# Optimization experiments

Measured on AMD Instinct MI355X. Metric: run time of the kernel, lower is better.

The kernel has to match this reference:

```python
import jax, jax.numpy as jnp
import numpy as np
from math import sqrt

D = 512        # output_dim (layer_dims[-1])
H = 4          # num_heads
ATN = D // H   # atn_dim = 128
BERT_D = 768
B = 32         # number of graph pairs
NP = 4096
NH = 4096


def setup_inputs() -> dict:
    key = jax.random.key(0)
    ks = jax.random.split(key, 20)
    inp = {
        'ctx_p': jax.random.normal(ks[0], (NP, D), jnp.float32),
        'ctx_h': jax.random.normal(ks[1], (NH, D), jnp.float32),
        'lhs_p': jax.random.normal(ks[2], (NP, BERT_D), jnp.float32),
        'lhs_h': jax.random.normal(ks[3], (NH, BERT_D), jnp.float32),
        'batch_p': jnp.sort(jax.random.randint(ks[4], (NP,), 0, B)).astype(jnp.int64),
        'batch_h': jnp.sort(jax.random.randint(ks[5], (NH,), 0, B)).astype(jnp.int64),
        # learned parameters (stored [in, out])
        'Wq': jax.random.normal(ks[6], (D, D), jnp.float32) * 0.02,
        'bq': jnp.zeros((D,), jnp.float32),
        'Wk': jax.random.normal(ks[7], (D, D), jnp.float32) * 0.02,
        'bk': jnp.zeros((D,), jnp.float32),
        'Wv': jax.random.normal(ks[8], (BERT_D, BERT_D), jnp.float32) * 0.02,
        'bv': jnp.zeros((BERT_D,), jnp.float32),
        'W1': jax.random.normal(ks[9], (D + BERT_D, 256), jnp.float32) * 0.02,
        'b1': jnp.zeros((256,), jnp.float32),
        'W2': jax.random.normal(ks[10], (256, 128), jnp.float32) * 0.02,
        'ln_g': jnp.ones((128,), jnp.float32),
        'ln_b': jnp.zeros((128,), jnp.float32),
        'Wc': jax.random.normal(ks[11], (128, 3), jnp.float32) * 0.02,
        'bc': jnp.zeros((3,), jnp.float32),
    }
    return inp


def reference(ctx_p, ctx_h, lhs_p, lhs_h, batch_p, batch_h,
              Wq, bq, Wk, bk, Wv, bv, W1, b1, W2, ln_g, ln_b, Wc, bc):
    # q/k projections; torch code does .view(-1, atn_dim, num_heads) -> head is fastest axis
    qs = (ctx_h @ Wq + bq).reshape(-1, ATN, H)          # [nh, atn, H]
    ks = (ctx_p @ Wk + bk).reshape(-1, ATN, H)          # [np, atn, H]
    vs = (lhs_p @ Wv + bv).reshape(-1, H, BERT_D // H)  # [np, H, 768/H]

    atn = jnp.einsum('ndh,mdh->nmh', qs, ks) / sqrt(ATN)  # [nh, np, H]
    # faithful to original: positions where batch ids MATCH are set to -1e10
    mask_same = batch_h[:, None] == batch_p[None, :]       # [nh, np]
    atn = jnp.where(mask_same[:, :, None], jnp.float32(-1e10), atn)
    atn = jax.nn.softmax(atn, axis=1)                      # softmax over premise words m

    attended = jnp.einsum('nmh,mhd->nhd', atn, vs).reshape(-1, BERT_D)  # [nh, 768]

    feats = jnp.concatenate([ctx_h, lhs_h - attended], axis=1)  # [nh, D+768]
    h1 = jax.nn.gelu(feats @ W1 + b1, approximate=False)
    h2 = h1 @ W2                                                # Linear no bias
    mu = h2.mean(axis=-1, keepdims=True)
    var = ((h2 - mu) ** 2).mean(axis=-1, keepdims=True)
    h2 = (h2 - mu) * jax.lax.rsqrt(var + 1e-5) * ln_g + ln_b    # LayerNorm(128)

    # global_mean_pool over batch_h
    pooled = jax.ops.segment_sum(h2, batch_h, num_segments=B)
    counts = jax.ops.segment_sum(jnp.ones((h2.shape[0], 1), h2.dtype), batch_h, num_segments=B)
    pooled = pooled / jnp.maximum(counts, 1.0)

    return pooled @ Wc + bc  # [B, 3]
```

## Files before the change

kernel.cpp:

```cpp
#include <hip/hip_runtime.h>
#include <hip/hip_bf16.h>
#include <math.h>

#define NP_N 4096
#define NH_N 4096
#define D_N 512
#define BERT_N 768
#define H_N 4
#define B_N 32
#define SCL2 0.12754245006257576f

typedef __attribute__((ext_vector_type(8))) short short8;
typedef __attribute__((ext_vector_type(4))) float f32x4;
typedef __attribute__((ext_vector_type(4))) unsigned short ush4;
typedef __attribute__((ext_vector_type(4))) unsigned int uivec4;
typedef unsigned short ushort_t;

__device__ __forceinline__ void gl_lds16(const void* g, void* l) {
    __builtin_amdgcn_global_load_lds((const __attribute__((address_space(1))) void*)g,
                                     (__attribute__((address_space(3))) void*)l, 16, 0, 0);
}
__device__ __forceinline__ unsigned short f2bu(float f) {
    __hip_bfloat16 b = __float2bfloat16(f);
    return *reinterpret_cast<unsigned short*>(&b);
}
__device__ __forceinline__ float b2f(unsigned short u) {
    union { unsigned int i; float f; } x; x.i = ((unsigned int)u) << 16; return x.f;
}
__device__ __forceinline__ unsigned int pkbf(float a, float b) {
    union { __hip_bfloat162 h; unsigned int u; } x;
    x.h.x = __float2bfloat16(a);
    x.h.y = __float2bfloat16(b);
    return x.u;
}
__device__ __forceinline__ unsigned int sxor(unsigned int v, int m) {
    return (unsigned int)__shfl_xor((int)v, m);
}

__device__ __forceinline__ short8 mkfrag(uint2 u, uint2 v, bool hi, bool godd) {
    unsigned ux32 = sxor(u.x, 32), uy32 = sxor(u.y, 32);
    unsigned vx32 = sxor(v.x, 32), vy32 = sxor(v.y, 32);
    unsigned ax = hi ? vx32 : u.x, bx = hi ? v.x : ux32;
    unsigned ay = hi ? vy32 : u.y, by = hi ? v.y : uy32;
    unsigned sbx = sxor(bx, 16), sax = sxor(ax, 16);
    unsigned sby = sxor(by, 16), say = sxor(ay, 16);
    uivec4 w;
    w.x = godd ? sbx : ax;
    w.y = godd ? sby : ay;
    w.z = godd ? bx : sax;
    w.w = godd ? by : say;
    return __builtin_bit_cast(short8, w);
}

#define EW_BLOCKS 512
__global__ __launch_bounds__(256) void convert_all(
    const float* __restrict__ ctx_h, const float* __restrict__ ctx_p,
    const float* __restrict__ lhs_p,
    const float* __restrict__ Wq, const float* __restrict__ Wk,
    const float* __restrict__ Wv, const float* __restrict__ W1,
    const float* __restrict__ bq, const float* __restrict__ bk,
    ushort_t* __restrict__ ctxp_bf, ushort_t* __restrict__ lhsp_bf,
    ushort_t* __restrict__ feats,
    ushort_t* __restrict__ Wqt, ushort_t* __restrict__ Wkt,
    ushort_t* __restrict__ Wvt, ushort_t* __restrict__ W1t,
    float* __restrict__ bqp, float* __restrict__ bkp)
{
    const int bid = blockIdx.x, t = threadIdx.x;
    if (bid < EW_BLOCKS) {
        const long N0 = 524288, N1 = 1048576, TOT = 1835008;
        for (long i = (long)bid * 256 + t; i < TOT; i += (long)EW_BLOCKS * 256) {
            float4 v; ush4 o;
            if (i < N0) {
                long k = i;
                v = ((const float4*)ctx_h)[k];
                o[0] = f2bu(v.x); o[1] = f2bu(v.y); o[2] = f2bu(v.z); o[3] = f2bu(v.w);
                long n = k >> 7, c4 = k & 127;
                ((ush4*)feats)[n * 320 + c4] = o;
            } else if (i < N1) {
                long k = i - N0;
                v = ((const float4*)ctx_p)[k];
                o[0] = f2bu(v.x); o[1] = f2bu(v.y); o[2] = f2bu(v.z); o[3] = f2bu(v.w);
                ((ush4*)ctxp_bf)[k] = o;
            } else {
                long k = i - N1;
                v = ((const float4*)lhs_p)[k];
                o[0] = f2bu(v.x); o[1] = f2bu(v.y); o[2] = f2bu(v.z); o[3] = f2bu(v.w);
                ((ush4*)lhsp_bf)[k] = o;
            }
        }
        if (bid == 0) {
            for (int n = t; n < 512; n += 256) {
                int np = (n & 3) * 128 + (n >> 2);
                bqp[np] = bq[n] * SCL2;
                bkp[np] = bk[n];
            }
        }
        return;
    }
    int tb = bid - EW_BLOCKS;
    const float* src; ushort_t* dst; int K, N, tile, perm; float wscl;
    if (tb < 64)       { src = Wq; dst = Wqt; K = 512;  N = 512; tile = tb;       perm = 1; wscl = SCL2; }
    else if (tb < 128) { src = Wk; dst = Wkt; K = 512;  N = 512; tile = tb - 64;  perm = 1; wscl = 1.f; }
    else if (tb < 272) { src = Wv; dst = Wvt; K = 768;  N = 768; tile = tb - 128; perm = 0; wscl = 1.f; }
    else               { src = W1; dst = W1t; K = 1280; N = 256; tile = tb - 272; perm = 0; wscl = 1.f; }
    int ntn = N >> 6;
    int k0 = (tile / ntn) * 64, n0 = (tile % ntn) * 64;
    __shared__ float tl[64][65];
#pragma unroll
    for (int i = 0; i < 16; i++) {
        int idx = t + i * 256; int r = idx >> 6, c = idx & 63;
        tl[r][c] = src[(size_t)(k0 + r) * N + n0 + c];
    }
    __syncthreads();
#pragma unroll
    for (int i = 0; i < 16; i++) {
        int idx = t + i * 256; int r = idx >> 6, c = idx & 63;
        int n = n0 + r;
        int nr = perm ? ((n & 3) * 128 + (n >> 2)) : n;
        dst[(size_t)nr * K + k0 + c] = f2bu(tl[c][r] * wscl);
    }
}

__global__ __launch_bounds__(256) void gemm_qkv(
    const ushort_t* __restrict__ feats, const ushort_t* __restrict__ ctxp,
    const ushort_t* __restrict__ Wqt, const ushort_t* __restrict__ Wkt,
    const ushort_t* __restrict__ Wvt, const ushort_t* __restrict__ lhsp,
    const float* __restrict__ bqp, const float* __restrict__ bkp,
    const float* __restrict__ bv,
    ushort_t* __restrict__ Qb, ushort_t* __restrict__ Kb,
    ushort_t* __restrict__ Vtb)
{
    int b = blockIdx.x;
    const ushort_t *A, *Bt; const float* bias; ushort_t* C;
    int lda, N, K, m0, n0, bias_row;
    if (b < 256) {
        A = feats; lda = 1280; Bt = Wqt; bias = bqp; C = Qb;
        N = 512; K = 512; bias_row = 0;
        n0 = (b & 7) * 64; m0 = (b >> 3) * 128;
    } else if (b < 512) {
        b -= 256;
        A = ctxp; lda = 512; Bt = Wkt; bias = bkp; C = Kb;
        N = 512; K = 512; bias_row = 0;
        n0 = (b & 7) * 64; m0 = (b >> 3) * 128;
    } else {
        b -= 512;
        A = Wvt; lda = 768; Bt = lhsp; bias = bv; C = Vtb;
        N = 4096; K = 768; bias_row = 1;
        n0 = (b & 63) * 64; m0 = (b >> 6) * 128;
    }
    const int nsteps = K >> 6;

    __shared__ ushort_t As[2][128 * 64];
    __shared__ ushort_t Bs[2][64 * 64];
    const int t = threadIdx.x, w = t >> 6, lane = t & 63;
    const int lq = lane & 15, g = lane >> 4;
    const int wm = w >> 1, wn = w & 1;

    f32x4 acc[4][2] = {};

    auto STAGE = [&](int buf, int k0) {
#pragma unroll
        for (int jj = 0; jj < 4; jj++) {
            int j = w * 4 + jj;
            int r = j * 8 + (lane >> 3);
            int c = (lane & 7) * 16;
            int cs = c ^ ((r & 7) << 4);
            gl_lds16((const char*)A + ((size_t)(m0 + r) * lda + k0) * 2 + cs,
                     (void*)&As[buf][j * 512]);
        }
#pragma unroll
        for (int jj = 0; jj < 2; jj++) {
            int j = w * 2 + jj;
            int r = j * 8 + (lane >> 3);
            int c = (lane & 7) * 16;
            int cs = c ^ ((r & 7) << 4);
            gl_lds16((const char*)Bt + ((size_t)(n0 + r) * K + k0) * 2 + cs,
                     (void*)&Bs[buf][j * 512]);
        }
    };

    STAGE(0, 0);
    asm volatile("s_waitcnt vmcnt(0)" ::: "memory");
    __builtin_amdgcn_s_barrier();
    int cur = 0;
    for (int s = 0; s < nsteps; s++) {
        if (s + 1 < nsteps) STAGE(cur ^ 1, (s + 1) * 64);
        const char* Ab = (const char*)&As[cur][0];
        const char* Bb = (const char*)&Bs[cur][0];
        const int swz = (lq & 7) << 4;
        short8 af[4][2], bfr[2][2];
#pragma unroll
        for (int mf = 0; mf < 4; mf++) {
            int r = wm * 64 + mf * 16 + lq;
#pragma unroll
            for (int ks = 0; ks < 2; ks++)
                af[mf][ks] = *(const short8*)(Ab + r * 128 + ((ks * 64 + g * 16) ^ swz));
        }
#pragma unroll
        for (int nf = 0; nf < 2; nf++) {
            int r = wn * 32 + nf * 16 + lq;
#pragma unroll
            for (int ks = 0; ks < 2; ks++)
                bfr[nf][ks] = *(const short8*)(Bb + r * 128 + ((ks * 64 + g * 16) ^ swz));
        }
        __builtin_amdgcn_s_setprio(1);
#pragma unroll
        for (int mf = 0; mf < 4; mf++)
#pragma unroll
            for (int nf = 0; nf < 2; nf++)
#pragma unroll
                for (int ks = 0; ks < 2; ks++)
                    acc[mf][nf] = __builtin_amdgcn_mfma_f32_16x16x32_bf16(
                        af[mf][ks], bfr[nf][ks], acc[mf][nf], 0, 0, 0);
        __builtin_amdgcn_s_setprio(0);
        asm volatile("s_waitcnt vmcnt(0)" ::: "memory");
        __builtin_amdgcn_s_barrier();
        cur ^= 1;
    }

#pragma unroll
    for (int mf = 0; mf < 4; mf++) {
#pragma unroll
        for (int nf = 0; nf < 2; nf++) {
            int ncol = n0 + wn * 32 + nf * 16 + lq;
            float bcol = bias_row ? 0.f : bias[ncol];
#pragma unroll
            for (int j = 0; j < 4; j++) {
                int mrow = m0 + wm * 64 + mf * 16 + 4 * g + j;
                float v = acc[mf][nf][j] + (bias_row ? bias[mrow] : bcol);
                C[(size_t)mrow * N + ncol] = f2bu(v);
            }
        }
    }
}

template<int TM, int TN>
__global__ __launch_bounds__(256) void gemm_mlp1(
    const ushort_t* __restrict__ A, int lda, const ushort_t* __restrict__ Bt,
    const float* __restrict__ bias, ushort_t* __restrict__ C,
    int M, int N, int K)
{
    constexpr int MF = TM / 32, NF = TN / 32;
    __shared__ ushort_t As[2][TM * 64];
    __shared__ ushort_t Bs[2][TN * 64];
    const int t = threadIdx.x, w = t >> 6, lane = t & 63;
    const int lq = lane & 15, g = lane >> 4;
    const int wm = w >> 1, wn = w & 1;
    const int n0 = blockIdx.x * TN, m0 = blockIdx.y * TM;
    const int nsteps = K >> 6;

    f32x4 acc[MF][NF] = {};

    auto STAGE = [&](int buf, int k0) {
#pragma unroll
        for (int jj = 0; jj < TM / 32; jj++) {
            int j = w * (TM / 32) + jj;
            int r = j * 8 + (lane >> 3);
            int c = (lane & 7) * 16;
            int cs = c ^ ((r & 7) << 4);
            gl_lds16((const char*)A + ((size_t)(m0 + r) * lda + k0) * 2 + cs,
                     (void*)&As[buf][j * 512]);
        }
#pragma unroll
        for (int jj = 0; jj < TN / 32; jj++) {
            int j = w * (TN / 32) + jj;
            int r = j * 8 + (lane >> 3);
            int c = (lane & 7) * 16;
            int cs = c ^ ((r & 7) << 4);
            gl_lds16((const char*)Bt + ((size_t)(n0 + r) * K + k0) * 2 + cs,
                     (void*)&Bs[buf][j * 512]);
        }
    };

    STAGE(0, 0);
    asm volatile("s_waitcnt vmcnt(0)" ::: "memory");
    __builtin_amdgcn_s_barrier();
    int cur = 0;
    for (int s = 0; s < nsteps; s++) {
        if (s + 1 < nsteps) STAGE(cur ^ 1, (s + 1) * 64);
        const char* Ab = (const char*)&As[cur][0];
        const char* Bb = (const char*)&Bs[cur][0];
        const int swz = (lq & 7) << 4;
        short8 af[MF][2], bfr[NF][2];
#pragma unroll
        for (int mf = 0; mf < MF; mf++) {
            int r = wm * (TM / 2) + mf * 16 + lq;
#pragma unroll
            for (int ks = 0; ks < 2; ks++)
                af[mf][ks] = *(const short8*)(Ab + r * 128 + ((ks * 64 + g * 16) ^ swz));
        }
#pragma unroll
        for (int nf = 0; nf < NF; nf++) {
            int r = wn * (TN / 2) + nf * 16 + lq;
#pragma unroll
            for (int ks = 0; ks < 2; ks++)
                bfr[nf][ks] = *(const short8*)(Bb + r * 128 + ((ks * 64 + g * 16) ^ swz));
        }
        __builtin_amdgcn_s_setprio(1);
#pragma unroll
        for (int mf = 0; mf < MF; mf++)
#pragma unroll
            for (int nf = 0; nf < NF; nf++)
#pragma unroll
                for (int ks = 0; ks < 2; ks++)
                    acc[mf][nf] = __builtin_amdgcn_mfma_f32_16x16x32_bf16(
                        af[mf][ks], bfr[nf][ks], acc[mf][nf], 0, 0, 0);
        __builtin_amdgcn_s_setprio(0);
        asm volatile("s_waitcnt vmcnt(0)" ::: "memory");
        __builtin_amdgcn_s_barrier();
        cur ^= 1;
    }

#pragma unroll
    for (int mf = 0; mf < MF; mf++) {
#pragma unroll
        for (int nf = 0; nf < NF; nf++) {
            int ncol = n0 + wn * (TN / 2) + nf * 16 + lq;
            float bcol = bias[ncol];
#pragma unroll
            for (int j = 0; j < 4; j++) {
                int mrow = m0 + wm * (TM / 2) + mf * 16 + 4 * g + j;
                float v = acc[mf][nf][j] + bcol;
                v = 0.5f * v * (1.f + erff(v * 0.70710678118654752f));
                C[(size_t)mrow * N + ncol] = f2bu(v);
            }
        }
    }
}

__global__ __launch_bounds__(512, 4) void attn_mfma(
    const ushort_t* __restrict__ Qb,
    const ushort_t* __restrict__ Kb,
    const ushort_t* __restrict__ Vtb,
    const int* __restrict__ batch_h, const int* __restrict__ batch_p,
    ushort_t* __restrict__ Opart,
    float* __restrict__ ml)
{
    const int bid = blockIdx.x;
    const int h = (bid & 7) >> 1;
    const int s = bid & 1;
    const int n0 = (bid >> 3) * 128;

    __shared__ __align__(16) char smem[81920];

    const int t = threadIdx.x;
    const int w = t >> 6;
    const int lane = t & 63, lq = lane & 15, g = lane >> 4;
    const int lqm = (lq & 7) << 4;
    const bool hi = lane >= 32;
    const bool godd = (lane & 16) != 0;

    char* Kt0 = smem;
    char* Kt1 = smem + 16384;
    char* Vt0 = smem + 32768;
    char* Vt1 = smem + 32768 + 24576;

    short8 qf[4];
    {
        const ushort_t* qrow = Qb + (size_t)(n0 + w * 16 + lq) * 512 + h * 128;
#pragma unroll
        for (int ks = 0; ks < 4; ks++)
            qf[ks] = *(const short8*)(qrow + ks * 32 + g * 8);
    }
    const int bhq = batch_h[n0 + w * 16 + lq];
    const int bh_lo = batch_h[n0 + w * 16];
    const int bh_hi = batch_h[n0 + w * 16 + 15];

    f32x4 Ofr[12];
#pragma unroll
    for (int nt = 0; nt < 12; nt++) Ofr[nt] = (f32x4){0.f, 0.f, 0.f, 0.f};
    float m_run = -1e30f, l_run = 0.f;

    const char* Kg = (const char*)Kb;
    const char* Vg = (const char*)Vtb;
    const int kb = s * 2048;

    int tlo = 0, thi = 0;
    if (lane < 32) {
        tlo = batch_p[kb + lane * 64];
        thi = batch_p[kb + lane * 64 + 63];
    }

    auto STAGE = [&](char* Kd, char* Vd, int m0k) {
#pragma unroll
        for (int jj = 0; jj < 2; jj++) {
            int j = w * 2 + jj;
            int r = j * 4 + (lane >> 4);
            int c = (lane & 15) * 16;
            gl_lds16(Kg + (size_t)(m0k + r) * 1024 + h * 256 + (c ^ ((r & 7) << 4)),
                     Kd + j * 1024);
        }
#pragma unroll
        for (int jj = 0; jj < 3; jj++) {
            int j = w * 3 + jj;
            int r = j * 8 + (lane >> 3);
            int c = (lane & 7) * 16;
            gl_lds16(Vg + ((size_t)(h * 192 + r) * 4096 + m0k) * 2 + (c ^ ((r & 7) << 4)),
                     Vd + j * 1024);
        }
    };

    STAGE(Kt0, Vt0, kb);
    asm volatile("s_waitcnt vmcnt(0)" ::: "memory");
    __builtin_amdgcn_s_barrier();
    int cur = 0;

    for (int tile = 0; tile < 32; tile++) {
        char* Kc = cur ? Kt1 : Kt0;
        char* Vc = cur ? Vt1 : Vt0;
        const int ktb = kb + tile * 64;
        const int klo = __shfl(tlo, tile);
        const int khi = __shfl(thi, tile);
        const bool allmask = (klo == khi) && (klo == bh_lo) && (bh_lo == bh_hi);
        const bool needmask = (klo <= bh_hi) && (khi >= bh_lo);

        if (tile + 1 < 32) STAGE(cur ? Kt0 : Kt1, cur ? Vt0 : Vt1, kb + (tile + 1) * 64);

        if (!allmask) {
            f32x4 S[4];
#pragma unroll
            for (int mt = 0; mt < 4; mt++) S[mt] = (f32x4){0.f, 0.f, 0.f, 0.f};
            __builtin_amdgcn_s_setprio(1);
#pragma unroll
            for (int mt = 0; mt < 4; mt++) {
                const char* rbase = Kc + (mt * 16 + lq) * 256;
#pragma unroll
                for (int ks = 0; ks < 4; ks++) {
                    short8 kf = *(const short8*)(rbase + ((ks * 64 + g * 16) ^ lqm));
                    S[mt] = __builtin_amdgcn_mfma_f32_16x16x32_bf16(kf, qf[ks], S[mt], 0, 0, 0);
                }
            }
            __builtin_amdgcn_s_setprio(0);

            float pmax = -1e30f;
            if (needmask) {
#pragma unroll
                for (int mt = 0; mt < 4; mt++) {
                    int4 bp = *(const int4*)&batch_p[ktb + mt * 16 + 4 * g];
                    float v0 = (bp.x == bhq) ? -1e9f : S[mt][0];
                    float v1 = (bp.y == bhq) ? -1e9f : S[mt][1];
                    float v2 = (bp.z == bhq) ? -1e9f : S[mt][2];
                    float v3 = (bp.w == bhq) ? -1e9f : S[mt][3];
                    S[mt][0] = v0; S[mt][1] = v1; S[mt][2] = v2; S[mt][3] = v3;
                    pmax = fmaxf(pmax, fmaxf(fmaxf(v0, v1), fmaxf(v2, v3)));
                }
            } else {
#pragma unroll
                for (int mt = 0; mt < 4; mt++)
                    pmax = fmaxf(pmax, fmaxf(fmaxf(S[mt][0], S[mt][1]),
                                             fmaxf(S[mt][2], S[mt][3])));
            }
            bool ng = __all(pmax <= m_run + 8.f);
            if (!ng) {
                float mq = fmaxf(pmax, m_run);
                mq = fmaxf(mq, __shfl_xor(mq, 16));
                mq = fmaxf(mq, __shfl_xor(mq, 32));
                float f = exp2f(m_run - mq);
                m_run = mq;
                l_run *= f;
                float fr0 = __shfl(f, 4 * g + 0);
                float fr1 = __shfl(f, 4 * g + 1);
                float fr2 = __shfl(f, 4 * g + 2);
                float fr3 = __shfl(f, 4 * g + 3);
#pragma unroll
                for (int nt = 0; nt < 12; nt++) {
                    Ofr[nt][0] *= fr0; Ofr[nt][1] *= fr1;
                    Ofr[nt][2] *= fr2; Ofr[nt][3] *= fr3;
                }
            }

            uint2 P2[4];
            float lsum = 0.f;
#pragma unroll
            for (int mt = 0; mt < 4; mt++) {
                float e0 = exp2f(S[mt][0] - m_run);
                float e1 = exp2f(S[mt][1] - m_run);
                float e2 = exp2f(S[mt][2] - m_run);
                float e3 = exp2f(S[mt][3] - m_run);
                lsum += (e0 + e1) + (e2 + e3);
                P2[mt].x = pkbf(e0, e1);
                P2[mt].y = pkbf(e2, e3);
            }
            l_run += lsum;

#pragma unroll
            for (int ks = 0; ks < 2; ks++) {
                short8 pf = mkfrag(P2[2 * ks], P2[2 * ks + 1], hi, godd);
                __builtin_amdgcn_s_setprio(1);
#pragma unroll
                for (int nt = 0; nt < 12; nt++) {
                    short8 vf = *(const short8*)(Vc + (nt * 16 + lq) * 128 + ((ks * 64 + g * 16) ^ lqm));
                    Ofr[nt] = __builtin_amdgcn_mfma_f32_16x16x32_bf16(pf, vf, Ofr[nt], 0, 0, 0);
                }
                __builtin_amdgcn_s_setprio(0);
            }
        }

        asm volatile("s_waitcnt vmcnt(0)" ::: "memory");
        __builtin_amdgcn_s_barrier();
        cur ^= 1;
    }

    float l = l_run;
    l += __shfl_xor(l, 16);
    l += __shfl_xor(l, 32);

    const size_t plane = (size_t)(s * 4 + h) * 4096;
    const int q0 = n0 + w * 16;
    if (g == 0) {
        ml[(plane + q0 + lq) * 2 + 0] = m_run;
        ml[(plane + q0 + lq) * 2 + 1] = l;
    }
#pragma unroll
    for (int nt = 0; nt < 12; nt++) {
#pragma unroll
        for (int j = 0; j < 4; j++)
            Opart[(plane + q0 + 4 * g + j) * 192 + nt * 16 + lq] = f2bu(Ofr[nt][j]);
    }
}

__global__ __launch_bounds__(256) void combine_feats(
    const ushort_t* __restrict__ Opart, const float* __restrict__ ml,
    const float* __restrict__ lhs_h, ushort_t* __restrict__ feats)
{
    const int t = threadIdx.x;
#pragma unroll
    for (int i = 0; i < 4; i++) {
        int q = blockIdx.x * 4 + i;
#pragma unroll
        for (int it = 0; it < 3; it++) {
            int c = t + it * 256;
            int h = c / 192, vd = c - h * 192;
            size_t i0 = (size_t)h * 4096 + q;
            size_t i1 = (size_t)(4 + h) * 4096 + q;
            float m0 = ml[i0 * 2], l0 = ml[i0 * 2 + 1];
            float m1 = ml[i1 * 2], l1 = ml[i1 * 2 + 1];
            float m = fmaxf(m0, m1);
            float e0 = exp2f(m0 - m), e1 = exp2f(m1 - m);
            float linv = 1.f / (l0 * e0 + l1 * e1);
            float O = (b2f(Opart[i0 * 192 + vd]) * e0 + b2f(Opart[i1 * 192 + vd]) * e1) * linv;
            feats[(size_t)q * 1280 + 512 + c] = f2bu(lhs_h[(size_t)q * 768 + c] - O);
        }
    }
}

__global__ __launch_bounds__(256) void h2_ln(
    const ushort_t* __restrict__ h1, const float* __restrict__ W2,
    const float* __restrict__ ln_g, const float* __restrict__ ln_b,
    float* __restrict__ h2out)
{
    const int n0 = blockIdx.x * 8;
    const int t = threadIdx.x;
    __shared__ float h1s[8][256];
    __shared__ float h2s[8][128];

#pragma unroll
    for (int i = 0; i < 8; i++) {
        int idx = t + i * 256; int r = idx >> 8, c = idx & 255;
        h1s[r][c] = b2f(h1[(size_t)(n0 + r) * 256 + c]);
    }
    __syncthreads();

    {
        int o2 = t & 127, gq = t >> 7;
        float acc[4] = {};
        for (int k4 = 0; k4 < 64; k4++) {
            float w0 = W2[(size_t)(k4 * 4 + 0) * 128 + o2];
            float w1 = W2[(size_t)(k4 * 4 + 1) * 128 + o2];
            float w2 = W2[(size_t)(k4 * 4 + 2) * 128 + o2];
            float w3 = W2[(size_t)(k4 * 4 + 3) * 128 + o2];
#pragma unroll
            for (int q = 0; q < 4; q++) {
                float4 hh = *(const float4*)&h1s[gq * 4 + q][k4 * 4];
                acc[q] += hh.x * w0 + hh.y * w1 + hh.z * w2 + hh.w * w3;
            }
        }
#pragma unroll
        for (int q = 0; q < 4; q++) h2s[gq * 4 + q][o2] = acc[q];
    }
    __syncthreads();

    {
        int wv = t >> 6, lane = t & 63;
#pragma unroll
        for (int sx = 0; sx < 2; sx++) {
            int nd = wv * 2 + sx;
            float x0 = h2s[nd][lane], x1 = h2s[nd][lane + 64];
            float sum = x0 + x1;
#pragma unroll
            for (int off = 32; off; off >>= 1) sum += __shfl_xor(sum, off);
            float mu = sum * (1.f / 128.f);
            float d0 = x0 - mu, d1 = x1 - mu;
            float s2 = d0 * d0 + d1 * d1;
#pragma unroll
            for (int off = 32; off; off >>= 1) s2 += __shfl_xor(s2, off);
            float rstd = rsqrtf(s2 * (1.f / 128.f) + 1e-5f);
            size_t base = (size_t)(n0 + nd) * 128;
            h2out[base + lane]      = d0 * rstd * ln_g[lane] + ln_b[lane];
            h2out[base + lane + 64] = d1 * rstd * ln_g[lane + 64] + ln_b[lane + 64];
        }
    }
}

__global__ __launch_bounds__(128) void pool_cls(
    const float* __restrict__ h2, const int* __restrict__ batch_h,
    const float* __restrict__ Wc, const float* __restrict__ bc,
    float* __restrict__ out)
{
    int b = blockIdx.x, t = threadIdx.x;
    __shared__ int bounds[2];
    if (t < 2) {
        int target = b + t;
        int lo = 0, hi = NH_N;
        while (lo < hi) {
            int mid = (lo + hi) >> 1;
            if (batch_h[mid] < target) lo = mid + 1; else hi = mid;
        }
        bounds[t] = lo;
    }
    __syncthreads();
    int s = bounds[0], e = bounds[1];
    float acc = 0.f;
    for (int n = s; n < e; n++) acc += h2[(size_t)n * 128 + t];
    float pooled = acc / fmaxf((float)(e - s), 1.f);
    __shared__ float red[128];
    for (int c = 0; c < 3; c++) {
        red[t] = pooled * Wc[t * 3 + c];
        __syncthreads();
        for (int off = 64; off > 0; off >>= 1) {
            if (t < off) red[t] += red[t + off];
            __syncthreads();
        }
        if (t == 0) out[b * 3 + c] = red[0] + bc[c];
        __syncthreads();
    }
}

extern "C" void kernel_launch(void* const* d_in, const int* in_sizes, int n_in,
                              void* d_out, int out_size, void* d_ws, size_t ws_size,
                              hipStream_t stream)
{
    const float* ctx_p  = (const float*)d_in[0];
    const float* ctx_h  = (const float*)d_in[1];
    const float* lhs_p  = (const float*)d_in[2];
    const float* lhs_h  = (const float*)d_in[3];
    const int*   batch_p = (const int*)d_in[4];
    const int*   batch_h = (const int*)d_in[5];
    const float* Wq = (const float*)d_in[6];
    const float* bq = (const float*)d_in[7];
    const float* Wk = (const float*)d_in[8];
    const float* bk = (const float*)d_in[9];
    const float* Wv = (const float*)d_in[10];
    const float* bv = (const float*)d_in[11];
    const float* W1 = (const float*)d_in[12];
    const float* b1 = (const float*)d_in[13];
    const float* W2 = (const float*)d_in[14];
    const float* ln_g = (const float*)d_in[15];
    const float* ln_b = (const float*)d_in[16];
    const float* Wc = (const float*)d_in[17];
    const float* bc = (const float*)d_in[18];
    float* out = (float*)d_out;

    ushort_t* u = (ushort_t*)d_ws;
    ushort_t* ctxp_bf = u;
    ushort_t* lhsp_bf = ctxp_bf + 2097152;
    ushort_t* Wqt  = lhsp_bf + 3145728;
    ushort_t* Wkt  = Wqt + 262144;
    ushort_t* Wvt  = Wkt + 262144;
    ushort_t* Opart = u;
    ushort_t* W1t  = Wvt + 589824;
    ushort_t* Qb   = W1t + 327680;
    ushort_t* Kb   = Qb + 2097152;
    ushort_t* Vtb  = Kb + 2097152;
    ushort_t* feats = Vtb + 3145728;
    ushort_t* h1   = feats + 5242880;
    float* ml  = (float*)(h1 + 1048576);
    float* h2  = ml + 65536;
    float* bqp = h2 + 524288;
    float* bkp = bqp + 512;

    convert_all<<<864, 256, 0, stream>>>(
        ctx_h, ctx_p, lhs_p, Wq, Wk, Wv, W1, bq, bk,
        ctxp_bf, lhsp_bf, feats, Wqt, Wkt, Wvt, W1t, bqp, bkp);

    gemm_qkv<<<896, 256, 0, stream>>>(
        feats, ctxp_bf, Wqt, Wkt, Wvt, lhsp_bf, bqp, bkp, bv, Qb, Kb, Vtb);

    attn_mfma<<<256, 512, 0, stream>>>(Qb, Kb, Vtb, batch_h, batch_p, Opart, ml);

    combine_feats<<<1024, 256, 0, stream>>>(Opart, ml, lhs_h, feats);

    gemm_mlp1<64, 64><<<dim3(4, 64), 256, 0, stream>>>(feats, 1280, W1t, b1, h1, NH_N, 256, 1280);

    h2_ln<<<512, 256, 0, stream>>>(h1, W2, ln_g, ln_b, h2);
    pool_cls<<<B_N, 128, 0, stream>>>(h2, batch_h, Wc, bc, out);
}
```

Baseline: 221.1 us.

## Split attention key range across warp groups with in-block split-K merge

Restructures the attention kernel so each block handles 64 queries, with its 8 warps arranged as 2 query-chunks by 4 key-splits. Each warp processes two 16-row query groups against a 32-key tile, sharing K/V fragments across both. The four key-split partial softmax states are merged through LDS at the end, and the grid doubles to 512 blocks. The aim is more parallelism and better reuse of each K/V fragment across queries. In exchange the double buffering is replaced by single-buffered staging with an extra barrier per tile, and a serial LDS reduction is added at the end.

```diff
diff --git a/kernel.cpp b/kernel.cpp
--- a/kernel.cpp
+++ b/kernel.cpp
@@ -338,184 +338,263 @@
 {
     const int bid = blockIdx.x;
     const int h = (bid & 7) >> 1;
-    const int s = bid & 1;
-    const int n0 = (bid >> 3) * 128;
+    const int outer = bid & 1;
+    const int n0 = (bid >> 3) * 64;
 
     __shared__ __align__(16) char smem[81920];
 
     const int t = threadIdx.x;
     const int w = t >> 6;
+    const int qc = w & 1;
+    const int si = w >> 1;
     const int lane = t & 63, lq = lane & 15, g = lane >> 4;
     const int lqm = (lq & 7) << 4;
     const bool hi = lane >= 32;
     const bool godd = (lane & 16) != 0;
 
-    char* Kt0 = smem;
-    char* Kt1 = smem + 16384;
-    char* Vt0 = smem + 32768;
-    char* Vt1 = smem + 32768 + 24576;
-
-    short8 qf[4];
-    {
-        const ushort_t* qrow = Qb + (size_t)(n0 + w * 16 + lq) * 512 + h * 128;
+    char* Kbuf = smem + si * 20480;
+    char* Vbuf = Kbuf + 8192;
+
+    short8 qf[2][4];
+    int bhq[2];
+#pragma unroll
+    for (int qg = 0; qg < 2; qg++) {
+        const ushort_t* qrow = Qb + (size_t)(n0 + qc * 32 + qg * 16 + lq) * 512 + h * 128;
 #pragma unroll
         for (int ks = 0; ks < 4; ks++)
-            qf[ks] = *(const short8*)(qrow + ks * 32 + g * 8);
-    }
-    const int bhq = batch_h[n0 + w * 16 + lq];
-    const int bh_lo = batch_h[n0 + w * 16];
-    const int bh_hi = batch_h[n0 + w * 16 + 15];
-
-    f32x4 Ofr[12];
-#pragma unroll
-    for (int nt = 0; nt < 12; nt++) Ofr[nt] = (f32x4){0.f, 0.f, 0.f, 0.f};
-    float m_run = -1e30f, l_run = 0.f;
+            qf[qg][ks] = *(const short8*)(qrow + ks * 32 + g * 8);
+        bhq[qg] = batch_h[n0 + qc * 32 + qg * 16 + lq];
+    }
+    const int bh_lo = batch_h[n0 + qc * 32];
+    const int bh_hi = batch_h[n0 + qc * 32 + 31];
+
+    f32x4 Ofr[2][12];
+#pragma unroll
+    for (int qg = 0; qg < 2; qg++)
+#pragma unroll
+        for (int nt = 0; nt < 12; nt++) Ofr[qg][nt] = (f32x4){0.f, 0.f, 0.f, 0.f};
+    float m_run[2] = {-1e30f, -1e30f}, l_run[2] = {0.f, 0.f};
 
     const char* Kg = (const char*)Kb;
     const char* Vg = (const char*)Vtb;
-    const int kb = s * 2048;
+    const int kb0 = (outer * 4 + si) * 512;
 
     int tlo = 0, thi = 0;
-    if (lane < 32) {
-        tlo = batch_p[kb + lane * 64];
-        thi = batch_p[kb + lane * 64 + 63];
-    }
-
-    auto STAGE = [&](char* Kd, char* Vd, int m0k) {
-#pragma unroll
-        for (int jj = 0; jj < 2; jj++) {
-            int j = w * 2 + jj;
+    if (lane < 16) {
+        tlo = batch_p[kb0 + lane * 32];
+        thi = batch_p[kb0 + lane * 32 + 31];
+    }
+    const int voff = ((lq >> 1) * 128) + ((((lq & 1) * 64) + g * 16) ^ (((lq >> 1) & 7) << 4));
+
+    auto STAGE = [&](int m0k) {
+#pragma unroll
+        for (int jj = 0; jj < 4; jj++) {
+            int j = qc * 4 + jj;
             int r = j * 4 + (lane >> 4);
-            int c = (lane & 15) * 16;
-            gl_lds16(Kg + (size_t)(m0k + r) * 1024 + h * 256 + (c ^ ((r & 7) << 4)),
-                     Kd + j * 1024);
-        }
-#pragma unroll
-        for (int jj = 0; jj < 3; jj++) {
-            int j = w * 3 + jj;
-            int r = j * 8 + (lane >> 3);
-            int c = (lane & 7) * 16;
-            gl_lds16(Vg + ((size_t)(h * 192 + r) * 4096 + m0k) * 2 + (c ^ ((r & 7) << 4)),
-                     Vd + j * 1024);
+            int c = ((lane & 15) * 16) ^ ((r & 7) << 4);
+            gl_lds16(Kg + (size_t)(m0k + r) * 1024 + h * 256 + c, Kbuf + j * 1024);
+        }
+#pragma unroll
+        for (int jj = 0; jj < 6; jj++) {
+            int j = qc * 6 + jj;
+            int r2 = j * 8 + (lane >> 3);
+            int raw = ((lane & 7) * 16) ^ ((r2 & 7) << 4);
+            int vd = 2 * r2 + (raw >> 6);
+            int kbyt = raw & 63;
+            gl_lds16(Vg + ((size_t)(h * 192 + vd) * 4096 + m0k) * 2 + kbyt, Vbuf + j * 1024);
         }
     };
 
-    STAGE(Kt0, Vt0, kb);
+    STAGE(kb0);
     asm volatile("s_waitcnt vmcnt(0)" ::: "memory");
     __builtin_amdgcn_s_barrier();
-    int cur = 0;
-
-    for (int tile = 0; tile < 32; tile++) {
-        char* Kc = cur ? Kt1 : Kt0;
-        char* Vc = cur ? Vt1 : Vt0;
-        const int ktb = kb + tile * 64;
+
+    for (int tile = 0; tile < 16; tile++) {
+        const int ktb = kb0 + tile * 32;
         const int klo = __shfl(tlo, tile);
         const int khi = __shfl(thi, tile);
         const bool allmask = (klo == khi) && (klo == bh_lo) && (bh_lo == bh_hi);
         const bool needmask = (klo <= bh_hi) && (khi >= bh_lo);
 
-        if (tile + 1 < 32) STAGE(cur ? Kt0 : Kt1, cur ? Vt0 : Vt1, kb + (tile + 1) * 64);
+        int4 bp0, bp1;
+        if (needmask && !allmask) {
+            bp0 = *(const int4*)&batch_p[ktb + 4 * g];
+            bp1 = *(const int4*)&batch_p[ktb + 16 + 4 * g];
+        }
 
         if (!allmask) {
-            f32x4 S[4];
-#pragma unroll
-            for (int mt = 0; mt < 4; mt++) S[mt] = (f32x4){0.f, 0.f, 0.f, 0.f};
+            f32x4 S[2][2];
+#pragma unroll
+            for (int qg = 0; qg < 2; qg++)
+#pragma unroll
+                for (int mt = 0; mt < 2; mt++) S[qg][mt] = (f32x4){0.f, 0.f, 0.f, 0.f};
             __builtin_amdgcn_s_setprio(1);
 #pragma unroll
-            for (int mt = 0; mt < 4; mt++) {
-                const char* rbase = Kc + (mt * 16 + lq) * 256;
+            for (int mt = 0; mt < 2; mt++) {
+                const char* rbase = Kbuf + (mt * 16 + lq) * 256;
 #pragma unroll
                 for (int ks = 0; ks < 4; ks++) {
                     short8 kf = *(const short8*)(rbase + ((ks * 64 + g * 16) ^ lqm));
-                    S[mt] = __builtin_amdgcn_mfma_f32_16x16x32_bf16(kf, qf[ks], S[mt], 0, 0, 0);
+                    S[0][mt] = __builtin_amdgcn_mfma_f32_16x16x32_bf16(kf, qf[0][ks], S[0][mt], 0, 0, 0);
+                    S[1][mt] = __builtin_amdgcn_mfma_f32_16x16x32_bf16(kf, qf[1][ks], S[1][mt], 0, 0, 0);
                 }
             }
             __builtin_amdgcn_s_setprio(0);
 
-            float pmax = -1e30f;
-            if (needmask) {
-#pragma unroll
-                for (int mt = 0; mt < 4; mt++) {
-                    int4 bp = *(const int4*)&batch_p[ktb + mt * 16 + 4 * g];
-                    float v0 = (bp.x == bhq) ? -1e9f : S[mt][0];
-                    float v1 = (bp.y == bhq) ? -1e9f : S[mt][1];
-                    float v2 = (bp.z == bhq) ? -1e9f : S[mt][2];
-                    float v3 = (bp.w == bhq) ? -1e9f : S[mt][3];
-                    S[mt][0] = v0; S[mt][1] = v1; S[mt][2] = v2; S[mt][3] = v3;
-                    pmax = fmaxf(pmax, fmaxf(fmaxf(v0, v1), fmaxf(v2, v3)));
+            float pmax[2];
+#pragma unroll
+            for (int qg = 0; qg < 2; qg++) {
+                float m = -1e30f;
+                if (needmask) {
+                    float v0 = (bp0.x == bhq[qg]) ? -1e9f : S[qg][0][0];
+                    float v1 = (bp0.y == bhq[qg]) ? -1e9f : S[qg][0][1];
+                    float v2 = (bp0.z == bhq[qg]) ? -1e9f : S[qg][0][2];
+                    float v3 = (bp0.w == bhq[qg]) ? -1e9f : S[qg][0][3];
+                    S[qg][0][0] = v0; S[qg][0][1] = v1; S[qg][0][2] = v2; S[qg][0][3] = v3;
+                    float u0 = (bp1.x == bhq[qg]) ? -1e9f : S[qg][1][0];
+                    float u1 = (bp1.y == bhq[qg]) ? -1e9f : S[qg][1][1];
+                    float u2 = (bp1.z == bhq[qg]) ? -1e9f : S[qg][1][2];
+                    float u3 = (bp1.w == bhq[qg]) ? -1e9f : S[qg][1][3];
+                    S[qg][1][0] = u0; S[qg][1][1] = u1; S[qg][1][2] = u2; S[qg][1][3] = u3;
+                    m = fmaxf(fmaxf(fmaxf(v0, v1), fmaxf(v2, v3)),
+                              fmaxf(fmaxf(u0, u1), fmaxf(u2, u3)));
+                } else {
+#pragma unroll
+                    for (int mt = 0; mt < 2; mt++)
+                        m = fmaxf(m, fmaxf(fmaxf(S[qg][mt][0], S[qg][mt][1]),
+                                           fmaxf(S[qg][mt][2], S[qg][mt][3])));
                 }
-            } else {
-#pragma unroll
-                for (int mt = 0; mt < 4; mt++)
-                    pmax = fmaxf(pmax, fmaxf(fmaxf(S[mt][0], S[mt][1]),
-                                             fmaxf(S[mt][2], S[mt][3])));
-            }
-            bool ng = __all(pmax <= m_run + 8.f);
+                pmax[qg] = m;
+            }
+            bool ng = __all((pmax[0] <= m_run[0] + 8.f) && (pmax[1] <= m_run[1] + 8.f));
             if (!ng) {
-                float mq = fmaxf(pmax, m_run);
-                mq = fmaxf(mq, __shfl_xor(mq, 16));
-                mq = fmaxf(mq, __shfl_xor(mq, 32));
-                float f = exp2f(m_run - mq);
-                m_run = mq;
-                l_run *= f;
-                float fr0 = __shfl(f, 4 * g + 0);
-                float fr1 = __shfl(f, 4 * g + 1);
-                float fr2 = __shfl(f, 4 * g + 2);
-                float fr3 = __shfl(f, 4 * g + 3);
-#pragma unroll
-                for (int nt = 0; nt < 12; nt++) {
-                    Ofr[nt][0] *= fr0; Ofr[nt][1] *= fr1;
-                    Ofr[nt][2] *= fr2; Ofr[nt][3] *= fr3;
+#pragma unroll
+                for (int qg = 0; qg < 2; qg++) {
+                    float mq = fmaxf(pmax[qg], m_run[qg]);
+                    mq = fmaxf(mq, __shfl_xor(mq, 16));
+                    mq = fmaxf(mq, __shfl_xor(mq, 32));
+                    float f = exp2f(m_run[qg] - mq);
+                    m_run[qg] = mq;
+                    l_run[qg] *= f;
+                    float fr0 = __shfl(f, 4 * g + 0);
+                    float fr1 = __shfl(f, 4 * g + 1);
+                    float fr2 = __shfl(f, 4 * g + 2);
+                    float fr3 = __shfl(f, 4 * g + 3);
+#pragma unroll
+                    for (int nt = 0; nt < 12; nt++) {
+                        Ofr[qg][nt][0] *= fr0; Ofr[qg][nt][1] *= fr1;
+                        Ofr[qg][nt][2] *= fr2; Ofr[qg][nt][3] *= fr3;
+                    }
                 }
             }
 
-            uint2 P2[4];
-            float lsum = 0.f;
-#pragma unroll
-            for (int mt = 0; mt < 4; mt++) {
-                float e0 = exp2f(S[mt][0] - m_run);
-                float e1 = exp2f(S[mt][1] - m_run);
-                float e2 = exp2f(S[mt][2] - m_run);
-                float e3 = exp2f(S[mt][3] - m_run);
-                lsum += (e0 + e1) + (e2 + e3);
-                P2[mt].x = pkbf(e0, e1);
-                P2[mt].y = pkbf(e2, e3);
-            }
-            l_run += lsum;
-
-#pragma unroll
-            for (int ks = 0; ks < 2; ks++) {
-                short8 pf = mkfrag(P2[2 * ks], P2[2 * ks + 1], hi, godd);
-                __builtin_amdgcn_s_setprio(1);
-#pragma unroll
-                for (int nt = 0; nt < 12; nt++) {
-                    short8 vf = *(const short8*)(Vc + (nt * 16 + lq) * 128 + ((ks * 64 + g * 16) ^ lqm));
-                    Ofr[nt] = __builtin_amdgcn_mfma_f32_16x16x32_bf16(pf, vf, Ofr[nt], 0, 0, 0);
+            uint2 P2[2][2];
+#pragma unroll
+            for (int qg = 0; qg < 2; qg++) {
+                float lsum = 0.f;
+#pragma unroll
+                for (int mt = 0; mt < 2; mt++) {
+                    float e0 = exp2f(S[qg][mt][0] - m_run[qg]);
+                    float e1 = exp2f(S[qg][mt][1] - m_run[qg]);
+                    float e2 = exp2f(S[qg][mt][2] - m_run[qg]);
+                    float e3 = exp2f(S[qg][mt][3] - m_run[qg]);
+                    lsum += (e0 + e1) + (e2 + e3);
+                    P2[qg][mt].x = pkbf(e0, e1);
+                    P2[qg][mt].y = pkbf(e2, e3);
                 }
-                __builtin_amdgcn_s_setprio(0);
-            }
-        }
-
+                l_run[qg] += lsum;
+            }
+
+            short8 pf0 = mkfrag(P2[0][0], P2[0][1], hi, godd);
+            short8 pf1 = mkfrag(P2[1][0], P2[1][1], hi, godd);
+            __builtin_amdgcn_s_setprio(1);
+#pragma unroll
+            for (int nt = 0; nt < 12; nt++) {
+                short8 vf = *(const short8*)(Vbuf + nt * 1024 + voff);
+                Ofr[0][nt] = __builtin_amdgcn_mfma_f32_16x16x32_bf16(pf0, vf, Ofr[0][nt], 0, 0, 0);
+                Ofr[1][nt] = __builtin_amdgcn_mfma_f32_16x16x32_bf16(pf1, vf, Ofr[1][nt], 0, 0, 0);
+            }
+            __builtin_amdgcn_s_setprio(0);
+        }
+
+        __builtin_amdgcn_s_barrier();
+        if (tile + 1 < 16) STAGE(ktb + 32);
         asm volatile("s_waitcnt vmcnt(0)" ::: "memory");
         __builtin_amdgcn_s_barrier();
-        cur ^= 1;
-    }
-
-    float l = l_run;
-    l += __shfl_xor(l, 16);
-    l += __shfl_xor(l, 32);
-
-    const size_t plane = (size_t)(s * 4 + h) * 4096;
-    const int q0 = n0 + w * 16;
-    if (g == 0) {
-        ml[(plane + q0 + lq) * 2 + 0] = m_run;
-        ml[(plane + q0 + lq) * 2 + 1] = l;
-    }
-#pragma unroll
-    for (int nt = 0; nt < 12; nt++) {
-#pragma unroll
-        for (int j = 0; j < 4; j++)
-            Opart[(plane + q0 + 4 * g + j) * 192 + nt * 16 + lq] = f2bu(Ofr[nt][j]);
+    }
+
+    float lt[2];
+#pragma unroll
+    for (int qg = 0; qg < 2; qg++) {
+        float l = l_run[qg];
+        l += __shfl_xor(l, 16);
+        l += __shfl_xor(l, 32);
+        lt[qg] = l;
+    }
+
+    float* mO = (float*)smem;
+    float* mls = (float*)(smem + 49152);
+    float m_acc[2] = {m_run[0], m_run[1]};
+    float l_acc[2] = {lt[0], lt[1]};
+
+    for (int p = 1; p < 4; p++) {
+        __syncthreads();
+        if (si == p) {
+            float* dst = mO + ((size_t)qc * 64 + lane) * 96;
+#pragma unroll
+            for (int qg = 0; qg < 2; qg++) {
+#pragma unroll
+                for (int nt = 0; nt < 12; nt++)
+                    *(f32x4*)(dst + qg * 48 + nt * 4) = Ofr[qg][nt];
+                if (g == 0) {
+                    mls[(((qc * 2 + qg) * 16) + lq) * 2 + 0] = m_run[qg];
+                    mls[(((qc * 2 + qg) * 16) + lq) * 2 + 1] = lt[qg];
+                }
+            }
+        }
+        __syncthreads();
+        if (si == 0) {
+            const float* srcO = mO + ((size_t)qc * 64 + lane) * 96;
+#pragma unroll
+            for (int qg = 0; qg < 2; qg++) {
+                float m1 = mls[(((qc * 2 + qg) * 16) + lq) * 2 + 0];
+                float l1 = mls[(((qc * 2 + qg) * 16) + lq) * 2 + 1];
+                float m = fmaxf(m_acc[qg], m1);
+                float a0 = exp2f(m_acc[qg] - m), a1 = exp2f(m1 - m);
+                l_acc[qg] = l_acc[qg] * a0 + l1 * a1;
+                m_acc[qg] = m;
+                float f0[4], f1[4];
+#pragma unroll
+                for (int j = 0; j < 4; j++) {
+                    f0[j] = __shfl(a0, 4 * g + j);
+                    f1[j] = __shfl(a1, 4 * g + j);
+                }
+#pragma unroll
+                for (int nt = 0; nt < 12; nt++) {
+                    f32x4 o1 = *(const f32x4*)(srcO + qg * 48 + nt * 4);
+#pragma unroll
+                    for (int j = 0; j < 4; j++)
+                        Ofr[qg][nt][j] = Ofr[qg][nt][j] * f0[j] + o1[j] * f1[j];
+                }
+            }
+        }
+    }
+
+    if (si == 0) {
+        const size_t plane = (size_t)(outer * 4 + h) * 4096;
+#pragma unroll
+        for (int qg = 0; qg < 2; qg++) {
+            int q0 = n0 + qc * 32 + qg * 16;
+            if (g == 0) {
+                ml[(plane + q0 + lq) * 2 + 0] = m_acc[qg];
+                ml[(plane + q0 + lq) * 2 + 1] = l_acc[qg];
+            }
+#pragma unroll
+            for (int nt = 0; nt < 12; nt++)
+#pragma unroll
+                for (int j = 0; j < 4; j++)
+                    Opart[(plane + q0 + 4 * g + j) * 192 + nt * 16 + lq] = f2bu(Ofr[qg][nt][j]);
+        }
     }
 }
 
@@ -686,7 +765,7 @@
     gemm_qkv<<<896, 256, 0, stream>>>(
         feats, ctxp_bf, Wqt, Wkt, Wvt, lhsp_bf, bqp, bkp, bv, Qb, Kb, Vtb);
 
-    attn_mfma<<<256, 512, 0, stream>>>(Qb, Kb, Vtb, batch_h, batch_p, Opart, ml);
+    attn_mfma<<<512, 512, 0, stream>>>(Qb, Kb, Vtb, batch_h, batch_p, Opart, ml);
 
     combine_feats<<<1024, 256, 0, stream>>>(Opart, ml, lhs_h, feats);
 
```

After: 621.1 us. 2.81x slower.
